# Performance work log

Measured on AMD Instinct MI355X. Metric: run time of the kernel, lower is better.

The kernel has to match this reference:

```python
import jax, jax.numpy as jnp
import numpy as np

B, C, H, W = 8, 320, 64, 64      # query feature map
S_KV, D_KV = 77, 1024            # key/value (text) tokens
HEADS, DIM_HEAD = 8, 64
INNER = HEADS * DIM_HEAD         # 512


def setup_inputs() -> dict:
    key = jax.random.key(0)
    ks = jax.random.split(key, 7)
    return {
        "query": jax.random.normal(ks[0], (B, C, H, W), dtype=jnp.float32),
        "key_value": jax.random.normal(ks[1], (B, S_KV, D_KV), dtype=jnp.float32),
        "Wq": jax.random.normal(ks[2], (C, INNER), dtype=jnp.float32) * (C ** -0.5),
        "Wk": jax.random.normal(ks[3], (D_KV, INNER), dtype=jnp.float32) * (D_KV ** -0.5),
        "Wv": jax.random.normal(ks[4], (D_KV, INNER), dtype=jnp.float32) * (D_KV ** -0.5),
        "Wo": jax.random.normal(ks[5], (INNER, C), dtype=jnp.float32) * (INNER ** -0.5),
        "bo": jnp.zeros((C,), dtype=jnp.float32),
    }


def reference(query, key_value, Wq, Wk, Wv, Wo, bo):
    b, c, h, w = query.shape
    n = h * w
    # [B,C,H,W] -> [B,N,C]
    q_flat = query.reshape(b, c, n).transpose(0, 2, 1)
    # projections, then split heads: [B, S, heads, dim_head]
    q = (q_flat @ Wq).reshape(b, n, HEADS, DIM_HEAD)
    k = (key_value @ Wk).reshape(b, S_KV, HEADS, DIM_HEAD)
    v = (key_value @ Wv).reshape(b, S_KV, HEADS, DIM_HEAD)
    scale = DIM_HEAD ** -0.5
    # attn logits: [B, heads, N, S_kv]
    logits = jnp.einsum('bnhd,bshd->bhns', q, k) * scale
    attn = jax.nn.softmax(logits, axis=-1)
    # weighted values -> merge heads: [B, N, inner]
    out = jnp.einsum('bhns,bshd->bnhd', attn, v).reshape(b, n, INNER)
    out = out @ Wo + bo  # dropout p=0.0 is identity
    # [B,N,C] -> [B,C,H,W]
    return out.transpose(0, 2, 1).reshape(b, c, h, w)
```

## Files before the change

### kernel.cpp

```cpp
#include <hip/hip_runtime.h>
#include <hip/hip_bf16.h>
#include <stdint.h>

#define BB     8
#define CC     320
#define NN     4096
#define SKV    77
#define HEADS  8
#define INNER  512
#define SCALE  0.125f

typedef float f32x4  __attribute__((ext_vector_type(4)));
typedef short bf16x8 __attribute__((ext_vector_type(8)));
typedef short s16x4  __attribute__((ext_vector_type(4)));

static __device__ __forceinline__ short f2bf(float f) {
  unsigned u = __float_as_uint(f);
  return (short)((u + 0x7fffu + ((u >> 16) & 1u)) >> 16);
}

static __device__ __forceinline__ void gll16(void* lds, const void* g) {
  auto gp = reinterpret_cast<const uint32_t __attribute__((address_space(1)))*>(
      reinterpret_cast<uintptr_t>(g));
  auto lp = reinterpret_cast<uint32_t __attribute__((address_space(3)))*>(
      reinterpret_cast<uintptr_t>(lds));
  __builtin_amdgcn_global_load_lds(gp, lp, 16, 0, 0);
}

__global__ __launch_bounds__(256) void prep_kernel(
    const float* __restrict__ kv, const float* __restrict__ Wk,
    const float* __restrict__ Wv, const float* __restrict__ Wq,
    const float* __restrict__ Wo, const float* __restrict__ query,
    short* __restrict__ kv_bf, short* __restrict__ Wk_t,
    short* __restrict__ Wv_t, short* __restrict__ Wq_t,
    short* __restrict__ Wo_t, short* __restrict__ X_bf,
    unsigned* __restrict__ zero_base) {
  __shared__ float T[64 * 65];
  const int blk = blockIdx.x, t = threadIdx.x;
  if (blk < 616) {
    const int base = blk * 1024;
    #pragma unroll
    for (int i = 0; i < 4; ++i) kv_bf[base + i*256 + t] = f2bf(kv[base + i*256 + t]);
    return;
  }
  if (blk >= 1392) {
    const int blk2 = blk - 1392;
    const int b = blk2 / 320, r = blk2 % 320;
    const int nt = r / 5, ct = r % 5;
    const int tl = t & 63, rb = t >> 6;
    #pragma unroll
    for (int i = 0; i < 16; ++i) {
      const int c = rb + i*4;
      T[c*65 + tl] = query[((size_t)(b*CC + ct*64 + c))*NN + nt*64 + tl];
    }
    __syncthreads();
    #pragma unroll
    for (int i = 0; i < 16; ++i) {
      const int n = rb + i*4;
      X_bf[((size_t)(b*NN + nt*64 + n))*CC + ct*64 + tl] = f2bf(T[tl*65 + n]);
    }
    return;
  }
  if (blk >= 952) {
    const int base = (blk - 952) * 1024;
    #pragma unroll
    for (int i = 0; i < 4; ++i) zero_base[base + i*256 + t] = 0u;
    return;
  }
  const float* src; short* dst; int RS, CS, kt, ct; float scl = 1.0f;
  if (blk < 872) {
    const int tile = blk - 616;
    const bool isK = tile < 128;
    const int tt = isK ? tile : tile - 128;
    src = isK ? Wk : Wv; dst = isK ? Wk_t : Wv_t;
    RS = 1024; CS = 512; kt = tt >> 3; ct = tt & 7;
  } else if (blk < 912) {
    const int tt = blk - 872;
    src = Wq; dst = Wq_t; RS = 320; CS = 512; kt = tt >> 3; ct = tt & 7;
    scl = SCALE;
  } else {
    const int tt = blk - 912;
    src = Wo; dst = Wo_t; RS = 512; CS = 320; kt = tt / 5; ct = tt % 5;
  }
  const int cl = t & 63, rb = t >> 6;
  #pragma unroll
  for (int i = 0; i < 16; ++i)
    T[(rb + i*4)*65 + cl] = src[(size_t)(kt*64 + rb + i*4)*CS + ct*64 + cl];
  __syncthreads();
  #pragma unroll
  for (int i = 0; i < 16; ++i) {
    const int nl = rb + i*4;
    dst[(size_t)(ct*64 + nl)*RS + kt*64 + cl] = f2bf(T[cl*65 + nl] * scl);
  }
}

__global__ __launch_bounds__(256) void kvproj_kernel(
    const short* __restrict__ kv_bf, const short* __restrict__ Wk_t,
    const short* __restrict__ Wv_t, short* __restrict__ K_ws,
    short* __restrict__ V_ws) {
  const int t = threadIdx.x, w = t >> 6, lane = t & 63;
  const int l15 = lane & 15, q = lane >> 4;
  const int m0 = (blockIdx.x * 4 + w) * 16;
  const int y = blockIdx.y;
  const bool isK = (y < 8);
  const int h = y & 7;
  const short* __restrict__ Wt = isK ? Wk_t : Wv_t;
  const int arow = (m0 + l15 < 616) ? (m0 + l15) : 615;

  const f32x4 z = {0.f, 0.f, 0.f, 0.f};
  f32x4 acc[4] = {z, z, z, z};
  for (int k0 = 0; k0 < 1024; k0 += 32) {
    const bf16x8 a = *(const bf16x8*)(kv_bf + arow*1024 + k0 + q*8);
    #pragma unroll
    for (int nt = 0; nt < 4; ++nt) {
      const int n = h*64 + nt*16 + l15;
      const bf16x8 bfr = *(const bf16x8*)(Wt + n*1024 + k0 + q*8);
      acc[nt] = __builtin_amdgcn_mfma_f32_16x16x32_bf16(a, bfr, acc[nt], 0, 0, 0);
    }
  }
  #pragma unroll
  for (int nt = 0; nt < 4; ++nt) {
    const int d = nt*16 + l15;
    #pragma unroll
    for (int r = 0; r < 4; ++r) {
      const int row = m0 + q*4 + r;
      if (row < 616) {
        const int b = (int)(((unsigned)row * 54472u) >> 22);
        const int s = row - b*77;
        if (isK) K_ws[((b*8 + h)*80 + s)*64 + d] = f2bf(acc[nt][r]);
        else     V_ws[((b*8 + h)*64 + d)*96 + s] = f2bf(acc[nt][r]);
      }
    }
  }
}

__global__ __launch_bounds__(256, 2) void qproj_kernel(
    const short* __restrict__ X_bf, const short* __restrict__ Wq_t,
    short* __restrict__ Q_ws) {
  const int t = threadIdx.x, w = t >> 6, lane = t & 63;
  const int l15 = lane & 15, q = lane >> 4;
  const int m0 = (blockIdx.x >> 1) * 128;
  const int n0 = (blockIdx.x & 1) * 256;
  const int wm = w & 1, wn = w >> 1;

  __shared__ short tile[12288];

  const f32x4 z = {0.f, 0.f, 0.f, 0.f};
  f32x4 acc[4][8];
  #pragma unroll
  for (int mt = 0; mt < 4; ++mt)
    #pragma unroll
    for (int nt = 0; nt < 8; ++nt) acc[mt][nt] = z;

  for (int it = 0; it < 10; ++it) {
    const int k0 = it * 32;
    if (it) __syncthreads();
    #pragma unroll
    for (int p = 0; p < 2; ++p) {
      const int f = p*256 + t, row = f >> 2, c4 = f & 3;
      gll16(tile + f*8, X_bf + (size_t)(m0 + row)*320 + k0 + c4*8);
    }
    #pragma unroll
    for (int p = 0; p < 4; ++p) {
      const int f = p*256 + t, row = f >> 2, c4 = f & 3;
      gll16(tile + 4096 + f*8, Wq_t + (size_t)(n0 + row)*320 + k0 + c4*8);
    }
    __syncthreads();
    bf16x8 a[4], bb[8];
    #pragma unroll
    for (int mt = 0; mt < 4; ++mt)
      a[mt] = *(const bf16x8*)(tile + (wm*64 + mt*16 + l15)*32 + q*8);
    #pragma unroll
    for (int nt = 0; nt < 8; ++nt)
      bb[nt] = *(const bf16x8*)(tile + 4096 + (wn*128 + nt*16 + l15)*32 + q*8);
    #pragma unroll
    for (int mt = 0; mt < 4; ++mt)
      #pragma unroll
      for (int nt = 0; nt < 8; ++nt)
        acc[mt][nt] = __builtin_amdgcn_mfma_f32_16x16x32_bf16(a[mt], bb[nt], acc[mt][nt], 0, 0, 0);
  }
  #pragma unroll
  for (int mt = 0; mt < 4; ++mt)
    #pragma unroll
    for (int r = 0; r < 4; ++r) {
      short* rowp = Q_ws + (size_t)(m0 + wm*64 + mt*16 + q*4 + r)*512 + n0 + wn*128;
      #pragma unroll
      for (int nt = 0; nt < 8; ++nt)
        rowp[nt*16 + l15] = f2bf(acc[mt][nt][r]);
    }
}

__global__ __launch_bounds__(256) void attncore_kernel(
    const short* __restrict__ Q_ws, const short* __restrict__ K_ws,
    const short* __restrict__ V_ws, short* __restrict__ O_ws) {
  const int t = threadIdx.x, w = t >> 6, lane = t & 63;
  const int unit = blockIdx.x * 4 + w;
  const int h = unit & 7;
  const int g = unit >> 3;
  const int b = g >> 7;
  const int n0 = (g & 127) * 32;
  const int l15 = lane & 15, q = lane >> 4;

  __shared__ short scr[4 * 32 * 104];
  short* scrw = scr + w * 32 * 104;
  for (int i = lane; i < 32*104/2; i += 64) ((unsigned*)scrw)[i] = 0u;

  const short* __restrict__ Kh = K_ws + (size_t)(b*8 + h) * 80 * 64;
  const short* __restrict__ Vh = V_ws + (size_t)(b*8 + h) * 64 * 96;
  size_t tokrow[2];
  #pragma unroll
  for (int nt = 0; nt < 2; ++nt) tokrow[nt] = (size_t)(b*NN + n0 + nt*16 + l15);

  const f32x4 z = {0.f, 0.f, 0.f, 0.f};
  f32x4 qk[2][5];
  #pragma unroll
  for (int nt = 0; nt < 2; ++nt)
    #pragma unroll
    for (int st = 0; st < 5; ++st) qk[nt][st] = z;
  #pragma unroll
  for (int f = 0; f < 2; ++f) {
    bf16x8 bq[2];
    #pragma unroll
    for (int nt = 0; nt < 2; ++nt)
      bq[nt] = *(const bf16x8*)(Q_ws + tokrow[nt]*512 + h*64 + f*32 + q*8);
    #pragma unroll
    for (int st = 0; st < 5; ++st) {
      const bf16x8 a = *(const bf16x8*)(Kh + (st*16 + l15)*64 + f*32 + q*8);
      #pragma unroll
      for (int nt = 0; nt < 2; ++nt)
        qk[nt][st] = __builtin_amdgcn_mfma_f32_16x16x32_bf16(a, bq[nt], qk[nt][st], 0, 0, 0);
    }
  }

  #pragma unroll
  for (int nt = 0; nt < 2; ++nt) {
    float mx = -1e30f;
    #pragma unroll
    for (int st = 0; st < 5; ++st)
      #pragma unroll
      for (int r = 0; r < 4; ++r) {
        const int s = st*16 + q*4 + r;
        const float vv = (s < SKV) ? qk[nt][st][r] : -1e30f;
        qk[nt][st][r] = vv;
        mx = fmaxf(mx, vv);
      }
    mx = fmaxf(mx, __shfl_xor(mx, 16));
    mx = fmaxf(mx, __shfl_xor(mx, 32));
    float sum = 0.f;
    #pragma unroll
    for (int st = 0; st < 5; ++st)
      #pragma unroll
      for (int r = 0; r < 4; ++r) {
        const int s = st*16 + q*4 + r;
        const float e = (s < SKV) ? __expf(qk[nt][st][r] - mx) : 0.f;
        qk[nt][st][r] = e;
        sum += e;
      }
    sum += __shfl_xor(sum, 16);
    sum += __shfl_xor(sum, 32);
    const float inv = 1.0f / sum;
    #pragma unroll
    for (int st = 0; st < 5; ++st) {
      s16x4 pv;
      #pragma unroll
      for (int r = 0; r < 4; ++r) pv[r] = f2bf(qk[nt][st][r] * inv);
      *(s16x4*)(scrw + (nt*16 + l15)*104 + st*16 + q*4) = pv;
    }
  }

  f32x4 ov[2][4];
  #pragma unroll
  for (int nt = 0; nt < 2; ++nt)
    #pragma unroll
    for (int dt = 0; dt < 4; ++dt) ov[nt][dt] = z;
  #pragma unroll
  for (int f = 0; f < 3; ++f) {
    bf16x8 bp[2];
    #pragma unroll
    for (int nt = 0; nt < 2; ++nt)
      bp[nt] = *(const bf16x8*)(scrw + (nt*16 + l15)*104 + f*32 + q*8);
    #pragma unroll
    for (int dt = 0; dt < 4; ++dt) {
      const bf16x8 a = *(const bf16x8*)(Vh + (dt*16 + l15)*96 + f*32 + q*8);
      #pragma unroll
      for (int nt = 0; nt < 2; ++nt)
        ov[nt][dt] = __builtin_amdgcn_mfma_f32_16x16x32_bf16(a, bp[nt], ov[nt][dt], 0, 0, 0);
    }
  }
  #pragma unroll
  for (int nt = 0; nt < 2; ++nt)
    #pragma unroll
    for (int dt = 0; dt < 4; ++dt) {
      s16x4 pv;
      #pragma unroll
      for (int r = 0; r < 4; ++r) pv[r] = f2bf(ov[nt][dt][r]);
      *(s16x4*)(O_ws + tokrow[nt]*512 + h*64 + dt*16 + q*4) = pv;
    }
}

__global__ __launch_bounds__(256) void outproj_kernel(
    const short* __restrict__ O_ws, const short* __restrict__ Wo_t,
    const float* __restrict__ bo, float* __restrict__ out) {
  const int t = threadIdx.x, w = t >> 6, lane = t & 63;
  const int l15 = lane & 15, q = lane >> 4;
  const int c0 = (blockIdx.x & 1) * 160;
  const int t0 = (blockIdx.x >> 1) * 128;
  const int wm = w & 1, wn = w >> 1;

  __shared__ short tile[9216];

  const f32x4 z = {0.f, 0.f, 0.f, 0.f};
  f32x4 acc[5][4];
  #pragma unroll
  for (int mt = 0; mt < 5; ++mt)
    #pragma unroll
    for (int nt = 0; nt < 4; ++nt) acc[mt][nt] = z;

  for (int it = 0; it < 16; ++it) {
    const int k0 = it * 32;
    if (it) __syncthreads();
    #pragma unroll
    for (int p = 0; p < 5; ++p) {
      const int f = p*256 + t;
      if (f < 1152) {
        const short* g;
        if (f < 640) {
          const int row = f >> 2, c4 = f & 3;
          g = Wo_t + (size_t)(c0 + row)*512 + k0 + c4*8;
        } else {
          const int f2 = f - 640, row = f2 >> 2, c4 = f2 & 3;
          g = O_ws + (size_t)(t0 + row)*512 + k0 + c4*8;
        }
        gll16(tile + f*8, g);
      }
    }
    __syncthreads();
    bf16x8 a[5], bb[4];
    #pragma unroll
    for (int mt = 0; mt < 5; ++mt)
      a[mt] = *(const bf16x8*)(tile + (wm*80 + mt*16 + l15)*32 + q*8);
    #pragma unroll
    for (int nt = 0; nt < 4; ++nt)
      bb[nt] = *(const bf16x8*)(tile + 5120 + (wn*64 + nt*16 + l15)*32 + q*8);
    #pragma unroll
    for (int mt = 0; mt < 5; ++mt)
      #pragma unroll
      for (int nt = 0; nt < 4; ++nt)
        acc[mt][nt] = __builtin_amdgcn_mfma_f32_16x16x32_bf16(a[mt], bb[nt], acc[mt][nt], 0, 0, 0);
  }
  const int b = t0 >> 12, n = t0 & 4095;
  #pragma unroll
  for (int mt = 0; mt < 5; ++mt)
    #pragma unroll
    for (int r = 0; r < 4; ++r) {
      const int c = c0 + wm*80 + mt*16 + q*4 + r;
      const float bv = bo[c];
      float* rowp = out + ((size_t)(b*CC + c))*NN + n + wn*64;
      #pragma unroll
      for (int nt = 0; nt < 4; ++nt)
        rowp[nt*16 + l15] = acc[mt][nt][r] + bv;
    }
}

extern "C" void kernel_launch(void* const* d_in, const int* in_sizes, int n_in,
                              void* d_out, int out_size, void* d_ws, size_t ws_size,
                              hipStream_t stream) {
  const float* query = (const float*)d_in[0];
  const float* kv    = (const float*)d_in[1];
  const float* Wq    = (const float*)d_in[2];
  const float* Wk    = (const float*)d_in[3];
  const float* Wv    = (const float*)d_in[4];
  const float* Wo    = (const float*)d_in[5];
  const float* bo    = (const float*)d_in[6];
  float* out = (float*)d_out;

  char* p = (char*)d_ws;
  short* K_ws  = (short*)(p);
  short* V_ws  = (short*)(p +   819200);
  short* Wq_t  = (short*)(p +  1802240);
  short* Wo_t  = (short*)(p +  2129920);
  short* Q_ws  = (short*)(p +  2457600);
  char* pb = p + 36012032;
  short* X_bf  = (short*)(pb);
  short* kv_bf = (short*)(pb + 20971520);
  short* Wk_t  = (short*)(pb + 22233088);
  short* Wv_t  = (short*)(pb + 23281664);
  short* O_ws  = (short*)(pb);

  prep_kernel<<<3952, 256, 0, stream>>>(kv, Wk, Wv, Wq, Wo, query, kv_bf,
                                        Wk_t, Wv_t, Wq_t, Wo_t, X_bf,
                                        (unsigned*)p);
  kvproj_kernel<<<dim3(10, 16), 256, 0, stream>>>(kv_bf, Wk_t, Wv_t, K_ws, V_ws);
  qproj_kernel<<<512, 256, 0, stream>>>(X_bf, Wq_t, Q_ws);
  attncore_kernel<<<2048, 256, 0, stream>>>(Q_ws, K_ws, V_ws, O_ws);
  outproj_kernel<<<512, 256, 0, stream>>>(O_ws, Wo_t, bo, out);
}
```

Before: 192.9 us.

## Double-buffer GEMM tiles, swizzle LDS layouts, stage K/V in LDS for attention

The q-projection and output-projection GEMMs now double-buffer their LDS tiles, prefetching the next k-slice before computing the current one. They also XOR-swizzle the column chunks to avoid LDS bank conflicts. The attention kernel is reorganised so each block handles one (batch, head, 256-token range) and loads that head's K and V once into LDS with swizzled layouts, instead of every wave reading them from global memory. V storage widens to 128 columns, and the workspace and prep-kernel grid are rearranged, which shrinks the zeroing region. This adds LDS pressure and may lower occupancy.

```diff
diff --git a/kernel.cpp b/kernel.cpp
--- a/kernel.cpp
+++ b/kernel.cpp
@@ -43,8 +43,8 @@
     for (int i = 0; i < 4; ++i) kv_bf[base + i*256 + t] = f2bf(kv[base + i*256 + t]);
     return;
   }
-  if (blk >= 1392) {
-    const int blk2 = blk - 1392;
+  if (blk >= 1208) {
+    const int blk2 = blk - 1208;
     const int b = blk2 / 320, r = blk2 % 320;
     const int nt = r / 5, ct = r % 5;
     const int tl = t & 63, rb = t >> 6;
@@ -110,11 +110,11 @@
   const f32x4 z = {0.f, 0.f, 0.f, 0.f};
   f32x4 acc[4] = {z, z, z, z};
   for (int k0 = 0; k0 < 1024; k0 += 32) {
-    const bf16x8 a = *(const bf16x8*)(kv_bf + arow*1024 + k0 + q*8);
+    const bf16x8 a = *(const bf16x8*)(kv_bf + (size_t)arow*1024 + k0 + q*8);
     #pragma unroll
     for (int nt = 0; nt < 4; ++nt) {
       const int n = h*64 + nt*16 + l15;
-      const bf16x8 bfr = *(const bf16x8*)(Wt + n*1024 + k0 + q*8);
+      const bf16x8 bfr = *(const bf16x8*)(Wt + (size_t)n*1024 + k0 + q*8);
       acc[nt] = __builtin_amdgcn_mfma_f32_16x16x32_bf16(a, bfr, acc[nt], 0, 0, 0);
     }
   }
@@ -127,8 +127,13 @@
       if (row < 616) {
         const int b = (int)(((unsigned)row * 54472u) >> 22);
         const int s = row - b*77;
-        if (isK) K_ws[((b*8 + h)*80 + s)*64 + d] = f2bf(acc[nt][r]);
-        else     V_ws[((b*8 + h)*64 + d)*96 + s] = f2bf(acc[nt][r]);
+        if (isK) {
+          const int u = (d >> 3) ^ (s & 7);
+          K_ws[(size_t)((b*8 + h)*80 + s)*64 + u*8 + (d & 7)] = f2bf(acc[nt][r]);
+        } else {
+          const int u = (s >> 3) ^ (d & 15);
+          V_ws[(size_t)((b*8 + h)*64 + d)*128 + u*8 + (s & 7)] = f2bf(acc[nt][r]);
+        }
       }
     }
   }
@@ -143,7 +148,24 @@
   const int n0 = (blockIdx.x & 1) * 256;
   const int wm = w & 1, wn = w >> 1;
 
-  __shared__ short tile[12288];
+  __shared__ short tile[2][12288];
+
+  auto stage = [&](int it, int bufi) {
+    short* buf = tile[bufi];
+    const int k0 = it * 32;
+    #pragma unroll
+    for (int p = 0; p < 2; ++p) {
+      const int f = p*256 + t, row = f >> 2, c4 = f & 3;
+      const int c4s = c4 ^ ((row & 3) ^ ((row >> 2) & 3));
+      gll16(buf + f*8, X_bf + (size_t)(m0 + row)*320 + k0 + c4s*8);
+    }
+    #pragma unroll
+    for (int p = 0; p < 4; ++p) {
+      const int f = p*256 + t, row = f >> 2, c4 = f & 3;
+      const int c4s = c4 ^ ((row & 3) ^ ((row >> 2) & 3));
+      gll16(buf + 4096 + f*8, Wq_t + (size_t)(n0 + row)*320 + k0 + c4s*8);
+    }
+  };
 
   const f32x4 z = {0.f, 0.f, 0.f, 0.f};
   f32x4 acc[4][8];
@@ -152,32 +174,25 @@
     #pragma unroll
     for (int nt = 0; nt < 8; ++nt) acc[mt][nt] = z;
 
+  stage(0, 0);
+  __syncthreads();
+  const int lperm = (l15 & 3) ^ ((l15 >> 2) & 3);
   for (int it = 0; it < 10; ++it) {
-    const int k0 = it * 32;
-    if (it) __syncthreads();
-    #pragma unroll
-    for (int p = 0; p < 2; ++p) {
-      const int f = p*256 + t, row = f >> 2, c4 = f & 3;
-      gll16(tile + f*8, X_bf + (size_t)(m0 + row)*320 + k0 + c4*8);
-    }
-    #pragma unroll
-    for (int p = 0; p < 4; ++p) {
-      const int f = p*256 + t, row = f >> 2, c4 = f & 3;
-      gll16(tile + 4096 + f*8, Wq_t + (size_t)(n0 + row)*320 + k0 + c4*8);
-    }
-    __syncthreads();
+    if (it + 1 < 10) stage(it + 1, (it + 1) & 1);
+    const short* buf = tile[it & 1];
     bf16x8 a[4], bb[8];
     #pragma unroll
     for (int mt = 0; mt < 4; ++mt)
-      a[mt] = *(const bf16x8*)(tile + (wm*64 + mt*16 + l15)*32 + q*8);
+      a[mt] = *(const bf16x8*)(buf + (wm*64 + mt*16 + l15)*32 + (q ^ lperm)*8);
     #pragma unroll
     for (int nt = 0; nt < 8; ++nt)
-      bb[nt] = *(const bf16x8*)(tile + 4096 + (wn*128 + nt*16 + l15)*32 + q*8);
+      bb[nt] = *(const bf16x8*)(buf + 4096 + (wn*128 + nt*16 + l15)*32 + (q ^ lperm)*8);
     #pragma unroll
     for (int mt = 0; mt < 4; ++mt)
       #pragma unroll
       for (int nt = 0; nt < 8; ++nt)
         acc[mt][nt] = __builtin_amdgcn_mfma_f32_16x16x32_bf16(a[mt], bb[nt], acc[mt][nt], 0, 0, 0);
+    if (it + 1 < 10) __syncthreads();
   }
   #pragma unroll
   for (int mt = 0; mt < 4; ++mt)
@@ -194,108 +209,126 @@
     const short* __restrict__ Q_ws, const short* __restrict__ K_ws,
     const short* __restrict__ V_ws, short* __restrict__ O_ws) {
   const int t = threadIdx.x, w = t >> 6, lane = t & 63;
-  const int unit = blockIdx.x * 4 + w;
-  const int h = unit & 7;
-  const int g = unit >> 3;
-  const int b = g >> 7;
-  const int n0 = (g & 127) * 32;
   const int l15 = lane & 15, q = lane >> 4;
-
+  const int b = blockIdx.x >> 7;
+  const int r7 = blockIdx.x & 127;
+  const int h = r7 >> 4;
+  const int rng = r7 & 15;
+
+  __shared__ short KL[80 * 64];
+  __shared__ short VL[64 * 128];
   __shared__ short scr[4 * 32 * 104];
-  short* scrw = scr + w * 32 * 104;
-  for (int i = lane; i < 32*104/2; i += 64) ((unsigned*)scrw)[i] = 0u;
-
-  const short* __restrict__ Kh = K_ws + (size_t)(b*8 + h) * 80 * 64;
-  const short* __restrict__ Vh = V_ws + (size_t)(b*8 + h) * 64 * 96;
-  size_t tokrow[2];
-  #pragma unroll
-  for (int nt = 0; nt < 2; ++nt) tokrow[nt] = (size_t)(b*NN + n0 + nt*16 + l15);
+
+  const short* __restrict__ Kg = K_ws + (size_t)(b*8 + h) * 80 * 64;
+  const short* __restrict__ Vg = V_ws + (size_t)(b*8 + h) * 64 * 128;
+  #pragma unroll
+  for (int p = 0; p < 3; ++p) {
+    const int L = p*256 + t;
+    if (L < 640) gll16(KL + L*8, Kg + L*8);
+  }
+  #pragma unroll
+  for (int p = 0; p < 4; ++p) {
+    const int L = p*256 + t;
+    gll16(VL + L*8, Vg + L*8);
+  }
+  short* scrw = scr + w * 3328;
+  for (int i = lane; i < 1664; i += 64) ((unsigned*)scrw)[i] = 0u;
+  __syncthreads();
 
   const f32x4 z = {0.f, 0.f, 0.f, 0.f};
-  f32x4 qk[2][5];
-  #pragma unroll
-  for (int nt = 0; nt < 2; ++nt)
-    #pragma unroll
-    for (int st = 0; st < 5; ++st) qk[nt][st] = z;
-  #pragma unroll
-  for (int f = 0; f < 2; ++f) {
-    bf16x8 bq[2];
+  for (int chunk = 0; chunk < 2; ++chunk) {
+    const int n0 = rng * 256 + w * 64 + chunk * 32;
+    size_t tokrow[2];
+    #pragma unroll
+    for (int nt = 0; nt < 2; ++nt) tokrow[nt] = (size_t)(b*NN + n0 + nt*16 + l15);
+
+    f32x4 qk[2][5];
     #pragma unroll
     for (int nt = 0; nt < 2; ++nt)
-      bq[nt] = *(const bf16x8*)(Q_ws + tokrow[nt]*512 + h*64 + f*32 + q*8);
-    #pragma unroll
-    for (int st = 0; st < 5; ++st) {
-      const bf16x8 a = *(const bf16x8*)(Kh + (st*16 + l15)*64 + f*32 + q*8);
+      #pragma unroll
+      for (int st = 0; st < 5; ++st) qk[nt][st] = z;
+    #pragma unroll
+    for (int f = 0; f < 2; ++f) {
+      bf16x8 bq[2];
       #pragma unroll
       for (int nt = 0; nt < 2; ++nt)
-        qk[nt][st] = __builtin_amdgcn_mfma_f32_16x16x32_bf16(a, bq[nt], qk[nt][st], 0, 0, 0);
-    }
-  }
-
-  #pragma unroll
-  for (int nt = 0; nt < 2; ++nt) {
-    float mx = -1e30f;
-    #pragma unroll
-    for (int st = 0; st < 5; ++st)
-      #pragma unroll
-      for (int r = 0; r < 4; ++r) {
-        const int s = st*16 + q*4 + r;
-        const float vv = (s < SKV) ? qk[nt][st][r] : -1e30f;
-        qk[nt][st][r] = vv;
-        mx = fmaxf(mx, vv);
-      }
-    mx = fmaxf(mx, __shfl_xor(mx, 16));
-    mx = fmaxf(mx, __shfl_xor(mx, 32));
-    float sum = 0.f;
-    #pragma unroll
-    for (int st = 0; st < 5; ++st)
-      #pragma unroll
-      for (int r = 0; r < 4; ++r) {
-        const int s = st*16 + q*4 + r;
-        const float e = (s < SKV) ? __expf(qk[nt][st][r] - mx) : 0.f;
-        qk[nt][st][r] = e;
-        sum += e;
-      }
-    sum += __shfl_xor(sum, 16);
-    sum += __shfl_xor(sum, 32);
-    const float inv = 1.0f / sum;
-    #pragma unroll
-    for (int st = 0; st < 5; ++st) {
-      s16x4 pv;
-      #pragma unroll
-      for (int r = 0; r < 4; ++r) pv[r] = f2bf(qk[nt][st][r] * inv);
-      *(s16x4*)(scrw + (nt*16 + l15)*104 + st*16 + q*4) = pv;
-    }
-  }
-
-  f32x4 ov[2][4];
-  #pragma unroll
-  for (int nt = 0; nt < 2; ++nt)
-    #pragma unroll
-    for (int dt = 0; dt < 4; ++dt) ov[nt][dt] = z;
-  #pragma unroll
-  for (int f = 0; f < 3; ++f) {
-    bf16x8 bp[2];
+        bq[nt] = *(const bf16x8*)(Q_ws + tokrow[nt]*512 + h*64 + f*32 + q*8);
+      #pragma unroll
+      for (int st = 0; st < 5; ++st) {
+        const int srow = st*16 + l15;
+        const bf16x8 a = *(const bf16x8*)(KL + srow*64 + ((f*4 + q) ^ (srow & 7))*8);
+        #pragma unroll
+        for (int nt = 0; nt < 2; ++nt)
+          qk[nt][st] = __builtin_amdgcn_mfma_f32_16x16x32_bf16(a, bq[nt], qk[nt][st], 0, 0, 0);
+      }
+    }
+
+    #pragma unroll
+    for (int nt = 0; nt < 2; ++nt) {
+      float mx = -1e30f;
+      #pragma unroll
+      for (int st = 0; st < 5; ++st)
+        #pragma unroll
+        for (int r = 0; r < 4; ++r) {
+          const int s = st*16 + q*4 + r;
+          const float vv = (s < SKV) ? qk[nt][st][r] : -1e30f;
+          qk[nt][st][r] = vv;
+          mx = fmaxf(mx, vv);
+        }
+      mx = fmaxf(mx, __shfl_xor(mx, 16));
+      mx = fmaxf(mx, __shfl_xor(mx, 32));
+      float sum = 0.f;
+      #pragma unroll
+      for (int st = 0; st < 5; ++st)
+        #pragma unroll
+        for (int r = 0; r < 4; ++r) {
+          const int s = st*16 + q*4 + r;
+          const float e = (s < SKV) ? __expf(qk[nt][st][r] - mx) : 0.f;
+          qk[nt][st][r] = e;
+          sum += e;
+        }
+      sum += __shfl_xor(sum, 16);
+      sum += __shfl_xor(sum, 32);
+      const float inv = 1.0f / sum;
+      #pragma unroll
+      for (int st = 0; st < 5; ++st) {
+        s16x4 pv;
+        #pragma unroll
+        for (int r = 0; r < 4; ++r) pv[r] = f2bf(qk[nt][st][r] * inv);
+        *(s16x4*)(scrw + (nt*16 + l15)*104 + st*16 + q*4) = pv;
+      }
+    }
+
+    f32x4 ov[2][4];
     #pragma unroll
     for (int nt = 0; nt < 2; ++nt)
-      bp[nt] = *(const bf16x8*)(scrw + (nt*16 + l15)*104 + f*32 + q*8);
-    #pragma unroll
-    for (int dt = 0; dt < 4; ++dt) {
-      const bf16x8 a = *(const bf16x8*)(Vh + (dt*16 + l15)*96 + f*32 + q*8);
+      #pragma unroll
+      for (int dt = 0; dt < 4; ++dt) ov[nt][dt] = z;
+    #pragma unroll
+    for (int f = 0; f < 3; ++f) {
+      bf16x8 bp[2];
       #pragma unroll
       for (int nt = 0; nt < 2; ++nt)
-        ov[nt][dt] = __builtin_amdgcn_mfma_f32_16x16x32_bf16(a, bp[nt], ov[nt][dt], 0, 0, 0);
-    }
-  }
-  #pragma unroll
-  for (int nt = 0; nt < 2; ++nt)
-    #pragma unroll
-    for (int dt = 0; dt < 4; ++dt) {
-      s16x4 pv;
-      #pragma unroll
-      for (int r = 0; r < 4; ++r) pv[r] = f2bf(ov[nt][dt][r]);
-      *(s16x4*)(O_ws + tokrow[nt]*512 + h*64 + dt*16 + q*4) = pv;
-    }
+        bp[nt] = *(const bf16x8*)(scrw + (nt*16 + l15)*104 + f*32 + q*8);
+      #pragma unroll
+      for (int dt = 0; dt < 4; ++dt) {
+        const int vrow = dt*16 + l15;
+        const bf16x8 a = *(const bf16x8*)(VL + vrow*128 + ((f*4 + q) ^ (vrow & 15))*8);
+        #pragma unroll
+        for (int nt = 0; nt < 2; ++nt)
+          ov[nt][dt] = __builtin_amdgcn_mfma_f32_16x16x32_bf16(a, bp[nt], ov[nt][dt], 0, 0, 0);
+      }
+    }
+    #pragma unroll
+    for (int nt = 0; nt < 2; ++nt)
+      #pragma unroll
+      for (int dt = 0; dt < 4; ++dt) {
+        s16x4 pv;
+        #pragma unroll
+        for (int r = 0; r < 4; ++r) pv[r] = f2bf(ov[nt][dt][r]);
+        *(s16x4*)(O_ws + tokrow[nt]*512 + h*64 + dt*16 + q*4) = pv;
+      }
+  }
 }
 
 __global__ __launch_bounds__(256) void outproj_kernel(
@@ -307,18 +340,11 @@
   const int t0 = (blockIdx.x >> 1) * 128;
   const int wm = w & 1, wn = w >> 1;
 
-  __shared__ short tile[9216];
-
-  const f32x4 z = {0.f, 0.f, 0.f, 0.f};
-  f32x4 acc[5][4];
-  #pragma unroll
-  for (int mt = 0; mt < 5; ++mt)
-    #pragma unroll
-    for (int nt = 0; nt < 4; ++nt) acc[mt][nt] = z;
-
-  for (int it = 0; it < 16; ++it) {
+  __shared__ short tile[2][9216];
+
+  auto stage = [&](int it, int bufi) {
+    short* buf = tile[bufi];
     const int k0 = it * 32;
-    if (it) __syncthreads();
     #pragma unroll
     for (int p = 0; p < 5; ++p) {
       const int f = p*256 + t;
@@ -326,27 +352,44 @@
         const short* g;
         if (f < 640) {
           const int row = f >> 2, c4 = f & 3;
-          g = Wo_t + (size_t)(c0 + row)*512 + k0 + c4*8;
+          const int c4s = c4 ^ ((row & 3) ^ ((row >> 2) & 3));
+          g = Wo_t + (size_t)(c0 + row)*512 + k0 + c4s*8;
         } else {
           const int f2 = f - 640, row = f2 >> 2, c4 = f2 & 3;
-          g = O_ws + (size_t)(t0 + row)*512 + k0 + c4*8;
+          const int c4s = c4 ^ ((row & 3) ^ ((row >> 2) & 3));
+          g = O_ws + (size_t)(t0 + row)*512 + k0 + c4s*8;
         }
-        gll16(tile + f*8, g);
-      }
-    }
-    __syncthreads();
+        gll16(buf + f*8, g);
+      }
+    }
+  };
+
+  const f32x4 z = {0.f, 0.f, 0.f, 0.f};
+  f32x4 acc[5][4];
+  #pragma unroll
+  for (int mt = 0; mt < 5; ++mt)
+    #pragma unroll
+    for (int nt = 0; nt < 4; ++nt) acc[mt][nt] = z;
+
+  stage(0, 0);
+  __syncthreads();
+  const int lperm = (l15 & 3) ^ ((l15 >> 2) & 3);
+  for (int it = 0; it < 16; ++it) {
+    if (it + 1 < 16) stage(it + 1, (it + 1) & 1);
+    const short* buf = tile[it & 1];
     bf16x8 a[5], bb[4];
     #pragma unroll
     for (int mt = 0; mt < 5; ++mt)
-      a[mt] = *(const bf16x8*)(tile + (wm*80 + mt*16 + l15)*32 + q*8);
+      a[mt] = *(const bf16x8*)(buf + (wm*80 + mt*16 + l15)*32 + (q ^ lperm)*8);
     #pragma unroll
     for (int nt = 0; nt < 4; ++nt)
-      bb[nt] = *(const bf16x8*)(tile + 5120 + (wn*64 + nt*16 + l15)*32 + q*8);
+      bb[nt] = *(const bf16x8*)(buf + 5120 + (wn*64 + nt*16 + l15)*32 + (q ^ lperm)*8);
     #pragma unroll
     for (int mt = 0; mt < 5; ++mt)
       #pragma unroll
       for (int nt = 0; nt < 4; ++nt)
         acc[mt][nt] = __builtin_amdgcn_mfma_f32_16x16x32_bf16(a[mt], bb[nt], acc[mt][nt], 0, 0, 0);
+    if (it + 1 < 16) __syncthreads();
   }
   const int b = t0 >> 12, n = t0 & 4095;
   #pragma unroll
@@ -377,21 +420,20 @@
   char* p = (char*)d_ws;
   short* K_ws  = (short*)(p);
   short* V_ws  = (short*)(p +   819200);
-  short* Wq_t  = (short*)(p +  1802240);
-  short* Wo_t  = (short*)(p +  2129920);
-  short* Q_ws  = (short*)(p +  2457600);
-  char* pb = p + 36012032;
-  short* X_bf  = (short*)(pb);
-  short* kv_bf = (short*)(pb + 20971520);
-  short* Wk_t  = (short*)(pb + 22233088);
-  short* Wv_t  = (short*)(pb + 23281664);
-  short* O_ws  = (short*)(pb);
-
-  prep_kernel<<<3952, 256, 0, stream>>>(kv, Wk, Wv, Wq, Wo, query, kv_bf,
+  short* Wq_t  = (short*)(p +  1867776);
+  short* Wo_t  = (short*)(p +  2195456);
+  short* kv_bf = (short*)(p +  2523136);
+  short* Wk_t  = (short*)(p +  3784704);
+  short* Wv_t  = (short*)(p +  4833280);
+  short* X_bf  = (short*)(p +  5881856);
+  short* Q_ws  = (short*)(p + 26853376);
+  short* O_ws  = (short*)(p + 60407808);
+
+  prep_kernel<<<3768, 256, 0, stream>>>(kv, Wk, Wv, Wq, Wo, query, kv_bf,
                                         Wk_t, Wv_t, Wq_t, Wo_t, X_bf,
-                                        (unsigned*)p);
+                                        (unsigned*)V_ws);
   kvproj_kernel<<<dim3(10, 16), 256, 0, stream>>>(kv_bf, Wk_t, Wv_t, K_ws, V_ws);
   qproj_kernel<<<512, 256, 0, stream>>>(X_bf, Wq_t, Q_ws);
-  attncore_kernel<<<2048, 256, 0, stream>>>(Q_ws, K_ws, V_ws, O_ws);
+  attncore_kernel<<<1024, 256, 0, stream>>>(Q_ws, K_ws, V_ws, O_ws);
   outproj_kernel<<<512, 256, 0, stream>>>(O_ws, Wo_t, bo, out);
 }
```

New measurement: 185.3 us. -3.9%, faster.
